# Kernel tuning notes

Hardware: AMD Instinct MI355X
Metric: run time of the kernel (lower is better)

## Reference

```python
import jax, jax.numpy as jnp
import numpy as np

N = 50000
E = 800000
H = 8
DH = 32  # hidden 256 / heads 8


def gat_layer(h, src, dst, W, a_src, a_dst, b):
    # h: [N, 256] -> per-head projected features [N, H, DH]
    hp = (h @ W).reshape(N, H, DH)
    # per-node attention logits for src/dst roles: [N, H]
    s_src = jnp.einsum('nhd,hd->nh', hp, a_src)
    s_dst = jnp.einsum('nhd,hd->nh', hp, a_dst)
    e = jax.nn.leaky_relu(s_src[src] + s_dst[dst], negative_slope=0.2)  # [Et, H]
    # segment softmax over incoming edges of each dst node
    m = jax.ops.segment_max(e, dst, num_segments=N)  # [N, H]
    ex = jnp.exp(e - m[dst])
    denom = jax.ops.segment_sum(ex, dst, num_segments=N)  # [N, H] (>0: self-loops)
    alpha = ex / denom[dst]  # [Et, H]
    out = jax.ops.segment_sum(alpha[:, :, None] * hp[src], dst, num_segments=N)
    return out.reshape(N, H * DH) + b


def han_forward(x, edges, proj_W, proj_b, gat_W, gat_asrc, gat_adst, gat_b,
                sem_W1, sem_b1, sem_W2, cls_W1, cls_b1, cls_W2, cls_b2):
    h0 = x @ proj_W + proj_b  # [N, 256]
    loop = jnp.arange(N, dtype=edges.dtype)
    embs = []
    for p in range(edges.shape[0]):  # 3 meta-paths (fixed, small)
        src = jnp.concatenate([edges[p, 0], loop])  # add self-loops (PyG default)
        dst = jnp.concatenate([edges[p, 1], loop])
        h = h0
        for l in range(2):  # 2 GAT layers per meta-path
            h = gat_layer(h, src, dst, gat_W[p, l], gat_asrc[p, l], gat_adst[p, l], gat_b[p, l])
            h = jax.nn.elu(h)  # dropout: eval-mode no-op
        embs.append(h)
    emb = jnp.stack(embs, axis=1)  # [N, P, 256]
    scores = (jnp.tanh(emb @ sem_W1 + sem_b1) @ sem_W2).squeeze(-1)  # [N, P]
    w = jax.nn.softmax(scores, axis=1)
    z = jnp.sum(emb * w[:, :, None], axis=1)  # [N, 256]
    hcls = jax.nn.relu(z @ cls_W1 + cls_b1)
    logits = hcls @ cls_W2 + cls_b2  # [N, 2]
    return logits


def setup_inputs() -> dict:
    key = jax.random.key(0)
    ks = jax.random.split(key, 16)
    s = 0.05
    return {
        'x': jax.random.normal(ks[0], (N, 128), jnp.float32),
        'edges': jax.random.randint(ks[1], (3, 2, E), 0, N, dtype=jnp.int32),
        'proj_W': jax.random.normal(ks[2], (128, 256), jnp.float32) * s,
        'proj_b': jnp.zeros((256,), jnp.float32),
        'gat_W': jax.random.normal(ks[3], (3, 2, 256, 256), jnp.float32) * s,
        'gat_asrc': jax.random.normal(ks[4], (3, 2, H, DH), jnp.float32) * s,
        'gat_adst': jax.random.normal(ks[5], (3, 2, H, DH), jnp.float32) * s,
        'gat_b': jnp.zeros((3, 2, 256), jnp.float32),
        'sem_W1': jax.random.normal(ks[6], (256, 128), jnp.float32) * s,
        'sem_b1': jnp.zeros((128,), jnp.float32),
        'sem_W2': jax.random.normal(ks[7], (128, 1), jnp.float32) * s,
        'cls_W1': jax.random.normal(ks[8], (256, 128), jnp.float32) * s,
        'cls_b1': jnp.zeros((128,), jnp.float32),
        'cls_W2': jax.random.normal(ks[9], (128, 2), jnp.float32) * s,
        'cls_b2': jnp.zeros((2,), jnp.float32),
    }


def reference(x, edges, proj_W, proj_b, gat_W, gat_asrc, gat_adst, gat_b,
              sem_W1, sem_b1, sem_W2, cls_W1, cls_b1, cls_W2, cls_b2):
    return han_forward(x, edges, proj_W, proj_b, gat_W, gat_asrc, gat_adst, gat_b,
                       sem_W1, sem_b1, sem_W2, cls_W1, cls_b1, cls_W2, cls_b2)
```

## Files before the change

### kernel.cpp

```cpp
#include <hip/hip_runtime.h>
#include <hip/hip_fp16.h>
#include <math.h>

#define N_NODES 50000
#define N_EDG   800000
#define NH      8
#define DH      32
#define HID     256
#define MAXD    64
#define EPB     4096
#define PROJ_FB 88
#define PROJ_EB (176*EPB)
#define G3_FB   69

typedef __attribute__((ext_vector_type(8))) short bf16x8;
typedef __attribute__((ext_vector_type(4))) float f32x4;

__device__ __forceinline__ unsigned short f2bf(float x) {
    unsigned u = __float_as_uint(x);
    u += 0x7FFF + ((u >> 16) & 1);
    return (unsigned short)(u >> 16);
}
__device__ __forceinline__ float bf2f(unsigned short h) {
    return __uint_as_float(((unsigned)h) << 16);
}
__device__ __forceinline__ float fastrcp(float x) {
    float r;
    asm("v_rcp_f32 %0, %1" : "=v"(r) : "v"(x));
    return r;
}
__device__ __forceinline__ void split8(const float4& a, const float4& b,
                                       uint4& hi, uint4& lo) {
    float v[8] = {a.x,a.y,a.z,a.w,b.x,b.y,b.z,b.w};
    unsigned short h[8], l[8];
    #pragma unroll
    for (int i = 0; i < 8; ++i) { h[i] = f2bf(v[i]); l[i] = f2bf(v[i] - bf2f(h[i])); }
// ... 34 lines not shown
        int dd[4], ss[4];
        #pragma unroll
        for (int j = 0; j < 4; ++j) {
            int e = base + (t * 4 + j) * 256;
            if (e < 3 * N_EDG) {
                int p = e / N_EDG, i = e - p * N_EDG;
                const int* src = edges + (size_t)p * 2 * N_EDG;
                int s = src[i], d = src[N_EDG + i];
                ss[j] = min(max(s, 0), N_NODES - 1);
                dd[j] = p * N_NODES + min(max(d, 0), N_NODES - 1);
            } else { ss[j] = -1; dd[j] = 0; }
        }
        int pos[4];
        #pragma unroll
        for (int j = 0; j < 4; ++j)
            if (ss[j] >= 0) pos[j] = atomicAdd(&cnt3[dd[j]], 1);
        #pragma unroll
        for (int j = 0; j < 4; ++j)
            if (ss[j] >= 0 && pos[j] < MAXD)
                slots3[(size_t)dd[j] * MAXD + pos[j]] = (unsigned short)ss[j];
    }
}

template<int NC, int ACT, int OUTMODE, int AMODE, int FILL>
__global__ __launch_bounds__(256)
void mfma_gemm_k(const float* __restrict__ A32p, const __half* __restrict__ A16p,
                 int lda,
                 const unsigned short* __restrict__ WThi,
                 const unsigned short* __restrict__ WTlo,
                 const float* __restrict__ bias,
                 float* __restrict__ C, __half* __restrict__ Ch,
                 int ldc, int M, int K,
                 const int* __restrict__ edges, int* __restrict__ cnt3,
                 unsigned short* __restrict__ slots3) {
    __shared__ unsigned short sAh[128*32], sAl[128*32], sBh[128*32], sBl[128*32];
    if constexpr (FILL) {
        const int gxk = (M + 127) >> 7;
        if ((int)blockIdx.x >= gxk) {
            fill_edges(edges, cnt3, slots3,
                       ((int)blockIdx.x - gxk) + PROJ_FB * (int)blockIdx.y, 0);
            return;
        }
    }
    const int tid  = threadIdx.x;
    const int lane = tid & 63;
    const int w    = tid >> 6;
    const int wr   = w >> 1, wc = w & 1;
    const int r0   = blockIdx.x * 128;
    const int c0   = blockIdx.y * 128;
    const int l15  = lane & 15, q = lane >> 4;

    const int cl8   = (((lane & 3) ^ ((lane >> 4) & 3)) << 3);
    const int lrow  = w*32 + (lane >> 2);
    const int gbrow0 = c0 + lrow, gbrow1 = c0 + lrow + 16;
    const int lbase = w * 1024;
    const int ldst  = lbase + lane * 8;

    const int srow = tid >> 2, slot = tid & 3;
    const size_t ga0 = (size_t)min(r0 + srow,      M - 1) * lda + slot * 8;
    const size_t ga1 = (size_t)min(r0 + srow + 64, M - 1) * lda + slot * 8;
    const int lda0 = srow*32 + ((slot ^ ((srow >> 2) & 3)) << 3);
    const int lda1 = lda0 + 64*32;

    f32x4 acc[4][4];
    #pragma unroll
    for (int i = 0; i < 4; ++i)
        #pragma unroll
        for (int j = 0; j < 4; ++j) acc[i][j] = (f32x4){0.f, 0.f, 0.f, 0.f};

    const int swzF = (l15 >> 2) & 3;
    const int qs   = ((q ^ swzF) << 3);

    const int nsteps = K >> 5;
    for (int s = 0; s < nsteps; ++s) {
        const int kc = s << 5;
        __syncthreads();
        uint4 h0, l0, h1, l1;
        if constexpr (AMODE == 0) {
            float4 f0a = *(const float4*)&A32p[ga0 + kc];
            float4 f0b = *(const float4*)&A32p[ga0 + kc + 4];
            float4 f1a = *(const float4*)&A32p[ga1 + kc];
            float4 f1b = *(const float4*)&A32p[ga1 + kc + 4];
            split8(f0a, f0b, h0, l0);
            split8(f1a, f1b, h1, l1);
        } else {
            uint4 r0v = *(const uint4*)&A16p[ga0 + kc];
            uint4 r1v = *(const uint4*)&A16p[ga1 + kc];
            h8_to_pair(r0v, h0, l0);
            h8_to_pair(r1v, h1, l1);
        }
        *(uint4*)&sAh[lda0] = h0; *(uint4*)&sAl[lda0] = l0;
        *(uint4*)&sAh[lda1] = h1; *(uint4*)&sAl[lda1] = l1;
        *(uint4*)&sBh[ldst]       = *(const uint4*)&WThi[(size_t)gbrow0*K + kc + cl8];
        *(uint4*)&sBh[ldst + 512] = *(const uint4*)&WThi[(size_t)gbrow1*K + kc + cl8];
        *(uint4*)&sBl[ldst]       = *(const uint4*)&WTlo[(size_t)gbrow0*K + kc + cl8];
        *(uint4*)&sBl[ldst + 512] = *(const uint4*)&WTlo[(size_t)gbrow1*K + kc + cl8];
        __syncthreads();

        bf16x8 fAh[4], fAl[4];
        #pragma unroll
        for (int t = 0; t < 4; ++t) {
            int ra = (wr*64 + t*16 + l15) * 32 + qs;
            fAh[t] = *(const bf16x8*)&sAh[ra];
            fAl[t] = *(const bf16x8*)&sAl[ra];
        }
        #pragma unroll
        for (int nt = 0; nt < 4; ++nt) {
            int rb = (wc*64 + nt*16 + l15) * 32 + qs;
            bf16x8 fBh = *(const bf16x8*)&sBh[rb];
            bf16x8 fBl = *(const bf16x8*)&sBl[rb];
            #pragma unroll
            for (int mt = 0; mt < 4; ++mt) {
                acc[mt][nt] = __builtin_amdgcn_mfma_f32_16x16x32_bf16(fAh[mt], fBh, acc[mt][nt], 0, 0, 0);
                acc[mt][nt] = __builtin_amdgcn_mfma_f32_16x16x32_bf16(fAh[mt], fBl, acc[mt][nt], 0, 0, 0);
                acc[mt][nt] = __builtin_amdgcn_mfma_f32_16x16x32_bf16(fAl[mt], fBh, acc[mt][nt], 0, 0, 0);
            }
        }
    }
    #pragma unroll
    for (int mt = 0; mt < 4; ++mt)
        #pragma unroll
        for (int nt = 0; nt < 4; ++nt) {
            int col = c0 + wc*64 + nt*16 + l15;
            float bb = bias ? bias[col] : 0.f;
            #pragma unroll
            for (int r = 0; r < 4; ++r) {
                int grow = r0 + wr*64 + mt*16 + q*4 + r;
                if (grow < M) {
                    float v = acc[mt][nt][r] + bb;
                    if (ACT == 1) {
                        float t = __expf(2.f * v);
                        v = 1.f - 2.f * fastrcp(1.f + t);
                    } else if (ACT == 2) v = fmaxf(v, 0.f);
                    size_t o = (size_t)grow * ldc + col;
                    if (OUTMODE == 2) Ch[o] = __float2half(v);
                    else              C[o] = v;
                }
            }
        }
}

template<int FILL>
__global__ __launch_bounds__(256)
void mfma_gemm3_k(const __half* __restrict__ A16p, int aoffz, int lda,
                  const unsigned short* __restrict__ WT, int l,
                  __half* __restrict__ hp3, int M,
                  const int* __restrict__ edges, int* __restrict__ cnt3,
                  unsigned short* __restrict__ slots3) {
    __shared__ unsigned short sAh[128*32], sAl[128*32], sBh[128*32], sBl[128*32];
    const int gx = (M + 127) >> 7;
    if constexpr (FILL) {
        if ((int)blockIdx.x >= gx) {
            fill_edges(edges, cnt3, slots3,
                       ((int)blockIdx.x - gx) + G3_FB * ((int)blockIdx.y + 2 * (int)blockIdx.z),
                       PROJ_EB);
            return;
        }
    }
    const int p = blockIdx.z;
    A16p += (size_t)p * aoffz;
    const unsigned short* WThi = WT + (size_t)(2*p + l) * 131072;
    const unsigned short* WTlo = WThi + 65536;
    __half* Ch = hp3 + (size_t)p * N_NODES * HID;
    const int K = HID;

    const int tid  = threadIdx.x;
    const int lane = tid & 63;
    const int w    = tid >> 6;
    const int wr   = w >> 1, wc = w & 1;
    const int r0   = blockIdx.x * 128;
    const int c0   = blockIdx.y * 128;
    const int l15  = lane & 15, q = lane >> 4;

    const int cl8   = (((lane & 3) ^ ((lane >> 4) & 3)) << 3);
    const int lrow  = w*32 + (lane >> 2);
    const int gbrow0 = c0 + lrow, gbrow1 = c0 + lrow + 16;
    const int lbase = w * 1024;
    const int ldst  = lbase + lane * 8;

    const int srow = tid >> 2, slot = tid & 3;
    const size_t ga0 = (size_t)min(r0 + srow,      M - 1) * lda + slot * 8;
    const size_t ga1 = (size_t)min(r0 + srow + 64, M - 1) * lda + slot * 8;
    const int lda0 = srow*32 + ((slot ^ ((srow >> 2) & 3)) << 3);
    const int lda1 = lda0 + 64*32;

    f32x4 acc[4][4];
    #pragma unroll
    for (int i = 0; i < 4; ++i)
        #pragma unroll
        for (int j = 0; j < 4; ++j) acc[i][j] = (f32x4){0.f, 0.f, 0.f, 0.f};

    const int swzF = (l15 >> 2) & 3;
    const int qs   = ((q ^ swzF) << 3);

    for (int s = 0; s < 8; ++s) {
        const int kc = s << 5;
        __syncthreads();
        uint4 r0v = *(const uint4*)&A16p[ga0 + kc];
        uint4 r1v = *(const uint4*)&A16p[ga1 + kc];
        uint4 h0, l0, h1, l1;
        h8_to_pair(r0v, h0, l0);
        h8_to_pair(r1v, h1, l1);
        *(uint4*)&sAh[lda0] = h0; *(uint4*)&sAl[lda0] = l0;
        *(uint4*)&sAh[lda1] = h1; *(uint4*)&sAl[lda1] = l1;
        *(uint4*)&sBh[ldst]       = *(const uint4*)&WThi[(size_t)gbrow0*K + kc + cl8];
        *(uint4*)&sBh[ldst + 512] = *(const uint4*)&WThi[(size_t)gbrow1*K + kc + cl8];
        *(uint4*)&sBl[ldst]       = *(const uint4*)&WTlo[(size_t)gbrow0*K + kc + cl8];
        *(uint4*)&sBl[ldst + 512] = *(const uint4*)&WTlo[(size_t)gbrow1*K + kc + cl8];
        __syncthreads();

        bf16x8 fAh[4], fAl[4];
        #pragma unroll
        for (int t = 0; t < 4; ++t) {
            int ra = (wr*64 + t*16 + l15) * 32 + qs;
            fAh[t] = *(const bf16x8*)&sAh[ra];
            fAl[t] = *(const bf16x8*)&sAl[ra];
        }
        #pragma unroll
        for (int nt = 0; nt < 4; ++nt) {
            int rb = (wc*64 + nt*16 + l15) * 32 + qs;
            bf16x8 fBh = *(const bf16x8*)&sBh[rb];
            bf16x8 fBl = *(const bf16x8*)&sBl[rb];
            #pragma unroll
            for (int mt = 0; mt < 4; ++mt) {
                acc[mt][nt] = __builtin_amdgcn_mfma_f32_16x16x32_bf16(fAh[mt], fBh, acc[mt][nt], 0, 0, 0);
                acc[mt][nt] = __builtin_amdgcn_mfma_f32_16x16x32_bf16(fAh[mt], fBl, acc[mt][nt], 0, 0, 0);
                acc[mt][nt] = __builtin_amdgcn_mfma_f32_16x16x32_bf16(fAl[mt], fBh, acc[mt][nt], 0, 0, 0);
            }
        }
    }
    #pragma unroll
    for (int mt = 0; mt < 4; ++mt)
        #pragma unroll
        for (int nt = 0; nt < 4; ++nt) {
            int col = c0 + wc*64 + nt*16 + l15;
            #pragma unroll
            for (int r = 0; r < 4; ++r) {
                int grow = r0 + wr*64 + mt*16 + q*4 + r;
                if (grow < M)
                    Ch[(size_t)grow * HID + col] = __float2half(acc[mt][nt][r]);
            }
        }
}

__global__ __launch_bounds__(256)
void cvtWall_k(const float* __restrict__ gatW, const float* __restrict__ projW,
               const float* __restrict__ semW1, const float* __restrict__ clsW1,
               unsigned short* __restrict__ WT) {
    int y = blockIdx.y;
    const float* W; int K, N;
    if (y < 6)       { W = gatW + (size_t)y * 65536; K = 256; N = 256; }
    else if (y == 6) { W = projW; K = 128; N = 256; }
    else if (y == 7) { W = semW1; K = 256; N = 128; }
    else             { W = clsW1; K = 256; N = 128; }
    int idx = blockIdx.x * 256 + threadIdx.x;
    if (idx >= K * N) return;
    unsigned short* hi = WT + (size_t)y * 131072;
    unsigned short* lo = hi + 65536;
    int k = idx / N, n = idx - k * N;
    float v = W[idx];
    unsigned short h = f2bf(v);
    hi[n * K + k] = h;
    lo[n * K + k] = f2bf(v - bf2f(h));
}

__global__ __launch_bounds__(256)
void attn_scores3_k(const __half* __restrict__ hp3,
                    const float* __restrict__ gatAs, const float* __restrict__ gatAd,
                    int l, float* __restrict__ ssrc3, float* __restrict__ sdst3) {
    int p = blockIdx.y;
    int gid = blockIdx.x * 256 + threadIdx.x;
    if (gid >= N_NODES * NH) return;
    int h = gid & 7;
    const __half2* hv = (const __half2*)(hp3 + (size_t)p * N_NODES * HID + (size_t)gid * DH);
    const float* a = gatAs + (2*p + l) * HID + h * DH;
    const float* d = gatAd + (2*p + l) * HID + h * DH;
    float ss = 0.f, sd = 0.f;
    #pragma unroll
    for (int j = 0; j < 8; ++j) {
        float4 av = ((const float4*)a)[j], dv = ((const float4*)d)[j];
        float2 f0 = __half22float2(hv[2*j]);
        float2 f1 = __half22float2(hv[2*j + 1]);
        ss += f0.x*av.x + f0.y*av.y + f1.x*av.z + f1.y*av.w;
        sd += f0.x*dv.x + f0.y*dv.y + f1.x*dv.z + f1.y*dv.w;
    }
    ssrc3[p * N_NODES * NH + gid] = ss;
    sdst3[p * N_NODES * NH + gid] = sd;
}

__global__ __launch_bounds__(256)
void zero_k(int* p, int n) { int i = blockIdx.x*256 + threadIdx.x; if (i < n) p[i] = 0; }

__global__ __launch_bounds__(256)
void agg3_k(const int* __restrict__ cnt3, const unsigned short* __restrict__ slots3,
            const float* __restrict__ ssrc3, const float* __restrict__ sdst3,
            const __half* __restrict__ hp3, const float* __restrict__ gatB, int l,
            __half* __restrict__ emb16) {
    const int p = blockIdx.y;
    int wid  = (blockIdx.x * blockDim.x + threadIdx.x) >> 6;
    int lane = threadIdx.x & 63;
    if (wid >= N_NODES) return;
    const int n = wid;
    const unsigned short* srcs = slots3 + ((size_t)p * N_NODES + n) * MAXD;
    const float* s_src = ssrc3 + p * N_NODES * NH;
    const float* s_dst = sdst3 + p * N_NODES * NH;
    const __half* hp = hp3 + (size_t)p * N_NODES * HID;
    const float* bias = gatB + (2*p + l) * HID;
    const int deg = min(cnt3[p * N_NODES + n], MAXD);

    const int sub = lane & 31, eo = lane >> 5;
    const int h2  = sub >> 2;
    const float sd2 = s_dst[n*NH + h2];
    const uint4* hp4 = (const uint4*)hp;
    float dn = 0.f;
    float a0=0.f,a1=0.f,a2=0.f,a3=0.f,a4=0.f,a5=0.f,a6=0.f,a7=0.f;

    int i = eo;
    for (; i + 6 < deg; i += 8) {
        const int s0 = srcs[i];
        const int s1 = srcs[i + 2];
        const int s2 = srcs[i + 4];
        const int s3 = srcs[i + 6];
        const float x0 = s_src[s0*NH + h2];
// ... 52 lines not shown
    a4 += __shfl_xor(a4, 32); a5 += __shfl_xor(a5, 32);
    a6 += __shfl_xor(a6, 32); a7 += __shfl_xor(a7, 32);
    if (lane < 32) {
        float evs = s_src[n*NH + h2] + sd2;
        evs = evs > 0.f ? evs : 0.2f * evs;
        float ws = __expf(evs);
        dn += ws;
        const uint4 rs = hp4[n*32 + sub];
        fmix2(a0, a1, rs.x, ws); fmix2(a2, a3, rs.y, ws);
        fmix2(a4, a5, rs.z, ws); fmix2(a6, a7, rs.w, ws);

        float rdn = fastrcp(dn);
        float v[8] = {a0,a1,a2,a3,a4,a5,a6,a7};
        const float4 b0 = *(const float4*)&bias[sub*8];
        const float4 b1 = *(const float4*)&bias[sub*8 + 4];
        v[0]=v[0]*rdn+b0.x; v[1]=v[1]*rdn+b0.y; v[2]=v[2]*rdn+b0.z; v[3]=v[3]*rdn+b0.w;
        v[4]=v[4]*rdn+b1.x; v[5]=v[5]*rdn+b1.y; v[6]=v[6]*rdn+b1.z; v[7]=v[7]*rdn+b1.w;
        unsigned short hh[8];
        #pragma unroll
        for (int k = 0; k < 8; ++k) {
            float e = v[k] > 0.f ? v[k] : (__expf(v[k]) - 1.f);
            hh[k] = __half_as_ushort(__float2half(e));
        }
        size_t o = (size_t)n * 768 + p * HID + sub * 8;
        *(uint4*)&emb16[o] = make_uint4(hh[0]|((unsigned)hh[1]<<16), hh[2]|((unsigned)hh[3]<<16),
                                        hh[4]|((unsigned)hh[5]<<16), hh[6]|((unsigned)hh[7]<<16));
    }
}

__global__ __launch_bounds__(256)
void score_z_k(const float* t, const float* __restrict__ W2,
               const __half* __restrict__ emb16, float* z) {
    int wid  = (blockIdx.x * blockDim.x + threadIdx.x) >> 6;
    int lane = threadIdx.x & 63;
    if (wid >= N_NODES) return;
    const int n = wid;
    float sc[3];
    #pragma unroll
    for (int p = 0; p < 3; ++p) {
        const float* tr = t + (size_t)(n*3 + p) * 128;
        float part = tr[lane] * W2[lane] + tr[64 + lane] * W2[64 + lane];
        #pragma unroll
        for (int o = 1; o < 64; o <<= 1) part += __shfl_xor(part, o);
        sc[p] = part;
    }
    float m  = fmaxf(sc[0], fmaxf(sc[1], sc[2]));
    float e0 = __expf(sc[0]-m), e1 = __expf(sc[1]-m), e2 = __expf(sc[2]-m);
    float rs = fastrcp(e0 + e1 + e2);
    e0 *= rs; e1 *= rs; e2 *= rs;
    const __half* er = emb16 + (size_t)n * 768;
    for (int c = lane; c < 256; c += 64) {
        float v0 = __half2float(er[c]);
        float v1 = __half2float(er[256 + c]);
        float v2 = __half2float(er[512 + c]);
        z[(size_t)n*384 + c] = e0*v0 + e1*v1 + e2*v2;
    }
}

__global__ __launch_bounds__(256)
void logits_k(const float* __restrict__ hcls, const float* __restrict__ W2,
              const float* __restrict__ b2, float* __restrict__ out) {
    int gid = blockIdx.x*256 + threadIdx.x;
    if (gid >= N_NODES * 2) return;
    int n = gid >> 1, o = gid & 1;
    const float* hr = hcls + (size_t)n * 128;
    float a = b2[o];
    #pragma unroll 4
    for (int j = 0; j < 128; ++j) a += hr[j] * W2[j*2 + o];
    out[gid] = a;
}

extern "C" void kernel_launch(void* const* d_in, const int* in_sizes, int n_in,
                              void* d_out, int out_size, void* d_ws, size_t ws_size,
                              hipStream_t stream) {
    (void)in_sizes; (void)n_in; (void)out_size; (void)ws_size;
    const float* x     = (const float*)d_in[0];
    const int*   edges = (const int*)  d_in[1];
    const float* projW = (const float*)d_in[2];
    const float* projb = (const float*)d_in[3];
// ... 1 lines not shown
    const float* gatAs = (const float*)d_in[5];
    const float* gatAd = (const float*)d_in[6];
    const float* gatB  = (const float*)d_in[7];
    const float* semW1 = (const float*)d_in[8];
    const float* semb1 = (const float*)d_in[9];
    const float* semW2 = (const float*)d_in[10];
    const float* clsW1 = (const float*)d_in[11];
    const float* clsb1 = (const float*)d_in[12];
    const float* clsW2 = (const float*)d_in[13];
    const float* clsb2 = (const float*)d_in[14];
    float* out = (float*)d_out;

    char* base = (char*)d_ws;
    const size_t PLANE = (size_t)N_NODES * HID * 2;
    __half* hp3   = (__half*)(base);
    __half* emb16 = (__half*)(base + 3*PLANE);
    __half* h016  = (__half*)(base + 6*PLANE);
    char* small = base + 7*PLANE;
    float* ssrc3 = (float*)small;
    float* sdst3 = ssrc3 + 3*(size_t)N_NODES*NH;
    int*   cnt3  = (int*)(sdst3 + 3*(size_t)N_NODES*NH);
    unsigned short* WT = (unsigned short*)(cnt3 + 3*N_NODES);
    unsigned short* slots3 = WT + 9*131072;
    float* tbuf = (float*)base;
    float* hcls = (float*)(base + 6*PLANE);

    dim3 blk(256);
    const int gx = (N_NODES + 127) / 128;

    cvtWall_k<<<dim3(256, 9), blk, 0, stream>>>(gatW, projW, semW1, clsW1, WT);
    zero_k  <<<(3*N_NODES+255)/256, blk, 0, stream>>>(cnt3, 3*N_NODES);

    mfma_gemm_k<256,0,2,0,1><<<dim3(gx + PROJ_FB, 2), blk, 0, stream>>>(
        x, nullptr, 128, WT + 6*131072, WT + 6*131072 + 65536, projb,
        nullptr, h016, 256, N_NODES, 128, edges, cnt3, slots3);

    for (int l = 0; l < 2; ++l) {
        if (l == 0)
            mfma_gemm3_k<1><<<dim3(gx + G3_FB, 2, 3), blk, 0, stream>>>(
                h016, 0, HID, WT, 0, hp3, N_NODES, edges, cnt3, slots3);
        else
            mfma_gemm3_k<0><<<dim3(gx, 2, 3), blk, 0, stream>>>(
                emb16, HID, 3*HID, WT, 1, hp3, N_NODES, edges, cnt3, slots3);
        attn_scores3_k<<<dim3((N_NODES*NH+255)/256, 3), blk, 0, stream>>>(
            hp3, gatAs, gatAd, l, ssrc3, sdst3);
        agg3_k<<<dim3((N_NODES*64)/256, 3), blk, 0, stream>>>(
            cnt3, slots3, ssrc3, sdst3, hp3, gatB, l, emb16);
    }

    mfma_gemm_k<128,1,0,1,0><<<dim3((150000+127)/128, 1), blk, 0, stream>>>(
        nullptr, emb16, 256, WT + 7*131072, WT + 7*131072 + 65536, semb1,
        tbuf, nullptr, 128, 150000, 256, nullptr, nullptr, nullptr);
    score_z_k<<<(N_NODES*64)/256, blk, 0, stream>>>(tbuf, semW2, emb16, tbuf);
    mfma_gemm_k<128,2,0,0,0><<<dim3(gx, 1), blk, 0, stream>>>(
        tbuf, nullptr, 384, WT + 8*131072, WT + 8*131072 + 65536, clsb1,
        hcls, nullptr, 128, N_NODES, 256, nullptr, nullptr, nullptr);
    logits_k<<<(N_NODES*2+255)/256, blk, 0, stream>>>(hcls, clsW2, clsb2, out);
}
```

Baseline: 984.2 us.

## Overlap per-metapath aggregation with GEMMs and fuse semantic weighting into classifier load

Breaks the batched three-metapath layer loop into per-metapath launches so each aggregation runs as extra blocks inside the next metapath's projection GEMM or semantic GEMM. This overlaps gather-heavy aggregation with MFMA work. The embedding layout changes from interleaved per-node to planar per-metapath. The semantic score kernel now writes only three softmax weights per node, and the classifier GEMM forms the weighted sum of the three embeddings while loading its A tile, which removes the z buffer write and read. The cost is more launches and heterogeneous blocks sharing one kernel, which can hurt occupancy or the balance of work across blocks.

```diff
diff --git a/kernel.cpp b/kernel.cpp
--- a/kernel.cpp
+++ b/kernel.cpp
@@ -12,6 +12,8 @@
 #define PROJ_FB 88
 #define PROJ_EB (176*EPB)
 #define G3_FB   69
+#define AGGB    12500
+#define AGGX3   6250
 
 typedef __attribute__((ext_vector_type(8))) short bf16x8;
 typedef __attribute__((ext_vector_type(4))) float f32x4;
@@ -92,283 +94,14 @@
     }
 }
 
-template<int NC, int ACT, int OUTMODE, int AMODE, int FILL>
-__global__ __launch_bounds__(256)
-void mfma_gemm_k(const float* __restrict__ A32p, const __half* __restrict__ A16p,
-                 int lda,
-                 const unsigned short* __restrict__ WThi,
-                 const unsigned short* __restrict__ WTlo,
-                 const float* __restrict__ bias,
-                 float* __restrict__ C, __half* __restrict__ Ch,
-                 int ldc, int M, int K,
-                 const int* __restrict__ edges, int* __restrict__ cnt3,
-                 unsigned short* __restrict__ slots3) {
-    __shared__ unsigned short sAh[128*32], sAl[128*32], sBh[128*32], sBl[128*32];
-    if constexpr (FILL) {
-        const int gxk = (M + 127) >> 7;
-        if ((int)blockIdx.x >= gxk) {
-            fill_edges(edges, cnt3, slots3,
-                       ((int)blockIdx.x - gxk) + PROJ_FB * (int)blockIdx.y, 0);
-            return;
-        }
-    }
-    const int tid  = threadIdx.x;
-    const int lane = tid & 63;
-    const int w    = tid >> 6;
-    const int wr   = w >> 1, wc = w & 1;
-    const int r0   = blockIdx.x * 128;
-    const int c0   = blockIdx.y * 128;
-    const int l15  = lane & 15, q = lane >> 4;
-
-    const int cl8   = (((lane & 3) ^ ((lane >> 4) & 3)) << 3);
-    const int lrow  = w*32 + (lane >> 2);
-    const int gbrow0 = c0 + lrow, gbrow1 = c0 + lrow + 16;
-    const int lbase = w * 1024;
-    const int ldst  = lbase + lane * 8;
-
-    const int srow = tid >> 2, slot = tid & 3;
-    const size_t ga0 = (size_t)min(r0 + srow,      M - 1) * lda + slot * 8;
-    const size_t ga1 = (size_t)min(r0 + srow + 64, M - 1) * lda + slot * 8;
-    const int lda0 = srow*32 + ((slot ^ ((srow >> 2) & 3)) << 3);
-    const int lda1 = lda0 + 64*32;
-
-    f32x4 acc[4][4];
-    #pragma unroll
-    for (int i = 0; i < 4; ++i)
-        #pragma unroll
-        for (int j = 0; j < 4; ++j) acc[i][j] = (f32x4){0.f, 0.f, 0.f, 0.f};
-
-    const int swzF = (l15 >> 2) & 3;
-    const int qs   = ((q ^ swzF) << 3);
-
-    const int nsteps = K >> 5;
-    for (int s = 0; s < nsteps; ++s) {
-        const int kc = s << 5;
-        __syncthreads();
-        uint4 h0, l0, h1, l1;
-        if constexpr (AMODE == 0) {
-            float4 f0a = *(const float4*)&A32p[ga0 + kc];
-            float4 f0b = *(const float4*)&A32p[ga0 + kc + 4];
-            float4 f1a = *(const float4*)&A32p[ga1 + kc];
-            float4 f1b = *(const float4*)&A32p[ga1 + kc + 4];
-            split8(f0a, f0b, h0, l0);
-            split8(f1a, f1b, h1, l1);
-        } else {
-            uint4 r0v = *(const uint4*)&A16p[ga0 + kc];
-            uint4 r1v = *(const uint4*)&A16p[ga1 + kc];
-            h8_to_pair(r0v, h0, l0);
-            h8_to_pair(r1v, h1, l1);
-        }
-        *(uint4*)&sAh[lda0] = h0; *(uint4*)&sAl[lda0] = l0;
-        *(uint4*)&sAh[lda1] = h1; *(uint4*)&sAl[lda1] = l1;
-        *(uint4*)&sBh[ldst]       = *(const uint4*)&WThi[(size_t)gbrow0*K + kc + cl8];
-        *(uint4*)&sBh[ldst + 512] = *(const uint4*)&WThi[(size_t)gbrow1*K + kc + cl8];
-        *(uint4*)&sBl[ldst]       = *(const uint4*)&WTlo[(size_t)gbrow0*K + kc + cl8];
-        *(uint4*)&sBl[ldst + 512] = *(const uint4*)&WTlo[(size_t)gbrow1*K + kc + cl8];
-        __syncthreads();
-
-        bf16x8 fAh[4], fAl[4];
-        #pragma unroll
-        for (int t = 0; t < 4; ++t) {
-            int ra = (wr*64 + t*16 + l15) * 32 + qs;
-            fAh[t] = *(const bf16x8*)&sAh[ra];
-            fAl[t] = *(const bf16x8*)&sAl[ra];
-        }
-        #pragma unroll
-        for (int nt = 0; nt < 4; ++nt) {
-            int rb = (wc*64 + nt*16 + l15) * 32 + qs;
-            bf16x8 fBh = *(const bf16x8*)&sBh[rb];
-            bf16x8 fBl = *(const bf16x8*)&sBl[rb];
-            #pragma unroll
-            for (int mt = 0; mt < 4; ++mt) {
-                acc[mt][nt] = __builtin_amdgcn_mfma_f32_16x16x32_bf16(fAh[mt], fBh, acc[mt][nt], 0, 0, 0);
-                acc[mt][nt] = __builtin_amdgcn_mfma_f32_16x16x32_bf16(fAh[mt], fBl, acc[mt][nt], 0, 0, 0);
-                acc[mt][nt] = __builtin_amdgcn_mfma_f32_16x16x32_bf16(fAl[mt], fBh, acc[mt][nt], 0, 0, 0);
-            }
-        }
-    }
-    #pragma unroll
-    for (int mt = 0; mt < 4; ++mt)
-        #pragma unroll
-        for (int nt = 0; nt < 4; ++nt) {
-            int col = c0 + wc*64 + nt*16 + l15;
-            float bb = bias ? bias[col] : 0.f;
-            #pragma unroll
-            for (int r = 0; r < 4; ++r) {
-                int grow = r0 + wr*64 + mt*16 + q*4 + r;
-                if (grow < M) {
-                    float v = acc[mt][nt][r] + bb;
-                    if (ACT == 1) {
-                        float t = __expf(2.f * v);
-                        v = 1.f - 2.f * fastrcp(1.f + t);
-                    } else if (ACT == 2) v = fmaxf(v, 0.f);
-                    size_t o = (size_t)grow * ldc + col;
-                    if (OUTMODE == 2) Ch[o] = __float2half(v);
-                    else              C[o] = v;
-                }
-            }
-        }
-}
-
-template<int FILL>
-__global__ __launch_bounds__(256)
-void mfma_gemm3_k(const __half* __restrict__ A16p, int aoffz, int lda,
-                  const unsigned short* __restrict__ WT, int l,
-                  __half* __restrict__ hp3, int M,
-                  const int* __restrict__ edges, int* __restrict__ cnt3,
-                  unsigned short* __restrict__ slots3) {
-    __shared__ unsigned short sAh[128*32], sAl[128*32], sBh[128*32], sBl[128*32];
-    const int gx = (M + 127) >> 7;
-    if constexpr (FILL) {
-        if ((int)blockIdx.x >= gx) {
-            fill_edges(edges, cnt3, slots3,
-                       ((int)blockIdx.x - gx) + G3_FB * ((int)blockIdx.y + 2 * (int)blockIdx.z),
-                       PROJ_EB);
-            return;
-        }
-    }
-    const int p = blockIdx.z;
-    A16p += (size_t)p * aoffz;
-    const unsigned short* WThi = WT + (size_t)(2*p + l) * 131072;
-    const unsigned short* WTlo = WThi + 65536;
-    __half* Ch = hp3 + (size_t)p * N_NODES * HID;
-    const int K = HID;
-
-    const int tid  = threadIdx.x;
-    const int lane = tid & 63;
-    const int w    = tid >> 6;
-    const int wr   = w >> 1, wc = w & 1;
-    const int r0   = blockIdx.x * 128;
-    const int c0   = blockIdx.y * 128;
-    const int l15  = lane & 15, q = lane >> 4;
-
-    const int cl8   = (((lane & 3) ^ ((lane >> 4) & 3)) << 3);
-    const int lrow  = w*32 + (lane >> 2);
-    const int gbrow0 = c0 + lrow, gbrow1 = c0 + lrow + 16;
-    const int lbase = w * 1024;
-    const int ldst  = lbase + lane * 8;
-
-    const int srow = tid >> 2, slot = tid & 3;
-    const size_t ga0 = (size_t)min(r0 + srow,      M - 1) * lda + slot * 8;
-    const size_t ga1 = (size_t)min(r0 + srow + 64, M - 1) * lda + slot * 8;
-    const int lda0 = srow*32 + ((slot ^ ((srow >> 2) & 3)) << 3);
-    const int lda1 = lda0 + 64*32;
-
-    f32x4 acc[4][4];
-    #pragma unroll
-    for (int i = 0; i < 4; ++i)
-        #pragma unroll
-        for (int j = 0; j < 4; ++j) acc[i][j] = (f32x4){0.f, 0.f, 0.f, 0.f};
-
-    const int swzF = (l15 >> 2) & 3;
-    const int qs   = ((q ^ swzF) << 3);
-
-    for (int s = 0; s < 8; ++s) {
-        const int kc = s << 5;
-        __syncthreads();
-        uint4 r0v = *(const uint4*)&A16p[ga0 + kc];
-        uint4 r1v = *(const uint4*)&A16p[ga1 + kc];
-        uint4 h0, l0, h1, l1;
-        h8_to_pair(r0v, h0, l0);
-        h8_to_pair(r1v, h1, l1);
-        *(uint4*)&sAh[lda0] = h0; *(uint4*)&sAl[lda0] = l0;
-        *(uint4*)&sAh[lda1] = h1; *(uint4*)&sAl[lda1] = l1;
-        *(uint4*)&sBh[ldst]       = *(const uint4*)&WThi[(size_t)gbrow0*K + kc + cl8];
-        *(uint4*)&sBh[ldst + 512] = *(const uint4*)&WThi[(size_t)gbrow1*K + kc + cl8];
-        *(uint4*)&sBl[ldst]       = *(const uint4*)&WTlo[(size_t)gbrow0*K + kc + cl8];
-        *(uint4*)&sBl[ldst + 512] = *(const uint4*)&WTlo[(size_t)gbrow1*K + kc + cl8];
-        __syncthreads();
-
-        bf16x8 fAh[4], fAl[4];
-        #pragma unroll
-        for (int t = 0; t < 4; ++t) {
-            int ra = (wr*64 + t*16 + l15) * 32 + qs;
-            fAh[t] = *(const bf16x8*)&sAh[ra];
-            fAl[t] = *(const bf16x8*)&sAl[ra];
-        }
-        #pragma unroll
-        for (int nt = 0; nt < 4; ++nt) {
-            int rb = (wc*64 + nt*16 + l15) * 32 + qs;
-            bf16x8 fBh = *(const bf16x8*)&sBh[rb];
-            bf16x8 fBl = *(const bf16x8*)&sBl[rb];
-            #pragma unroll
-            for (int mt = 0; mt < 4; ++mt) {
-                acc[mt][nt] = __builtin_amdgcn_mfma_f32_16x16x32_bf16(fAh[mt], fBh, acc[mt][nt], 0, 0, 0);
-                acc[mt][nt] = __builtin_amdgcn_mfma_f32_16x16x32_bf16(fAh[mt], fBl, acc[mt][nt], 0, 0, 0);
-                acc[mt][nt] = __builtin_amdgcn_mfma_f32_16x16x32_bf16(fAl[mt], fBh, acc[mt][nt], 0, 0, 0);
-            }
-        }
-    }
-    #pragma unroll
-    for (int mt = 0; mt < 4; ++mt)
-        #pragma unroll
-        for (int nt = 0; nt < 4; ++nt) {
-            int col = c0 + wc*64 + nt*16 + l15;
-            #pragma unroll
-            for (int r = 0; r < 4; ++r) {
-                int grow = r0 + wr*64 + mt*16 + q*4 + r;
-                if (grow < M)
-                    Ch[(size_t)grow * HID + col] = __float2half(acc[mt][nt][r]);
-            }
-        }
-}
-
-__global__ __launch_bounds__(256)
-void cvtWall_k(const float* __restrict__ gatW, const float* __restrict__ projW,
-               const float* __restrict__ semW1, const float* __restrict__ clsW1,
-               unsigned short* __restrict__ WT) {
-    int y = blockIdx.y;
-    const float* W; int K, N;
-    if (y < 6)       { W = gatW + (size_t)y * 65536; K = 256; N = 256; }
-    else if (y == 6) { W = projW; K = 128; N = 256; }
-    else if (y == 7) { W = semW1; K = 256; N = 128; }
-    else             { W = clsW1; K = 256; N = 128; }
-    int idx = blockIdx.x * 256 + threadIdx.x;
-    if (idx >= K * N) return;
-    unsigned short* hi = WT + (size_t)y * 131072;
-    unsigned short* lo = hi + 65536;
-    int k = idx / N, n = idx - k * N;
-    float v = W[idx];
-    unsigned short h = f2bf(v);
-    hi[n * K + k] = h;
-    lo[n * K + k] = f2bf(v - bf2f(h));
-}
-
-__global__ __launch_bounds__(256)
-void attn_scores3_k(const __half* __restrict__ hp3,
-                    const float* __restrict__ gatAs, const float* __restrict__ gatAd,
-                    int l, float* __restrict__ ssrc3, float* __restrict__ sdst3) {
-    int p = blockIdx.y;
-    int gid = blockIdx.x * 256 + threadIdx.x;
-    if (gid >= N_NODES * NH) return;
-    int h = gid & 7;
-    const __half2* hv = (const __half2*)(hp3 + (size_t)p * N_NODES * HID + (size_t)gid * DH);
-    const float* a = gatAs + (2*p + l) * HID + h * DH;
-    const float* d = gatAd + (2*p + l) * HID + h * DH;
-    float ss = 0.f, sd = 0.f;
-    #pragma unroll
-    for (int j = 0; j < 8; ++j) {
-        float4 av = ((const float4*)a)[j], dv = ((const float4*)d)[j];
-        float2 f0 = __half22float2(hv[2*j]);
-        float2 f1 = __half22float2(hv[2*j + 1]);
-        ss += f0.x*av.x + f0.y*av.y + f1.x*av.z + f1.y*av.w;
-        sd += f0.x*dv.x + f0.y*dv.y + f1.x*dv.z + f1.y*dv.w;
-    }
-    ssrc3[p * N_NODES * NH + gid] = ss;
-    sdst3[p * N_NODES * NH + gid] = sd;
-}
-
-__global__ __launch_bounds__(256)
-void zero_k(int* p, int n) { int i = blockIdx.x*256 + threadIdx.x; if (i < n) p[i] = 0; }
-
-__global__ __launch_bounds__(256)
-void agg3_k(const int* __restrict__ cnt3, const unsigned short* __restrict__ slots3,
-            const float* __restrict__ ssrc3, const float* __restrict__ sdst3,
-            const __half* __restrict__ hp3, const float* __restrict__ gatB, int l,
-            __half* __restrict__ emb16) {
-    const int p = blockIdx.y;
-    int wid  = (blockIdx.x * blockDim.x + threadIdx.x) >> 6;
-    int lane = threadIdx.x & 63;
+__device__ __forceinline__ void agg_worker(
+    int fb, int p, int l,
+    const int* __restrict__ cnt3, const unsigned short* __restrict__ slots3,
+    const float* __restrict__ ssrc3, const float* __restrict__ sdst3,
+    const __half* __restrict__ hp3, const float* __restrict__ gatB,
+    __half* __restrict__ emb16) {
+    const int wid  = fb * 4 + ((int)threadIdx.x >> 6);
+    const int lane = threadIdx.x & 63;
     if (wid >= N_NODES) return;
     const int n = wid;
     const unsigned short* srcs = slots3 + ((size_t)p * N_NODES + n) * MAXD;
@@ -467,15 +200,342 @@
             float e = v[k] > 0.f ? v[k] : (__expf(v[k]) - 1.f);
             hh[k] = __half_as_ushort(__float2half(e));
         }
-        size_t o = (size_t)n * 768 + p * HID + sub * 8;
+        size_t o = ((size_t)p * N_NODES + n) * HID + sub * 8;
         *(uint4*)&emb16[o] = make_uint4(hh[0]|((unsigned)hh[1]<<16), hh[2]|((unsigned)hh[3]<<16),
                                         hh[4]|((unsigned)hh[5]<<16), hh[6]|((unsigned)hh[7]<<16));
     }
 }
 
 __global__ __launch_bounds__(256)
-void score_z_k(const float* t, const float* __restrict__ W2,
-               const __half* __restrict__ emb16, float* z) {
+void agg1_k(const int* __restrict__ cnt3, const unsigned short* __restrict__ slots3,
+            const float* __restrict__ ssrc3, const float* __restrict__ sdst3,
+            const __half* __restrict__ hp3, const float* __restrict__ gatB,
+            int p, int l, __half* __restrict__ emb16) {
+    agg_worker(blockIdx.x, p, l, cnt3, slots3, ssrc3, sdst3, hp3, gatB, emb16);
+}
+
+template<int NC, int ACT, int OUTMODE, int AMODE, int FILL, int AGG>
+__global__ __launch_bounds__(256)
+void mfma_gemm_k(const float* __restrict__ A32p, const __half* __restrict__ A16p,
+                 int lda,
+                 const unsigned short* __restrict__ WThi,
+                 const unsigned short* __restrict__ WTlo,
+                 const float* __restrict__ bias,
+                 float* __restrict__ C, __half* __restrict__ Ch,
+                 int ldc, int M, int K,
+                 const int* __restrict__ edges, int* __restrict__ cnt3,
+                 unsigned short* __restrict__ slots3,
+                 const float* __restrict__ ssrc3, const float* __restrict__ sdst3,
+                 const float* __restrict__ gatB, const __half* __restrict__ aggHp,
+                 __half* __restrict__ aggEmb, int aggp, int aggl,
+                 const float* __restrict__ w4z) {
+    __shared__ unsigned short sAh[128*32], sAl[128*32], sBh[128*32], sBl[128*32];
+    const int gxk = (M + 127) >> 7;
+    if constexpr (FILL) {
+        if ((int)blockIdx.x >= gxk) {
+            fill_edges(edges, cnt3, slots3,
+                       ((int)blockIdx.x - gxk) + PROJ_FB * (int)blockIdx.y, 0);
+            return;
+        }
+    }
+    if constexpr (AGG) {
+        if ((int)blockIdx.x >= gxk) {
+            agg_worker((int)blockIdx.x - gxk, aggp, aggl,
+                       cnt3, slots3, ssrc3, sdst3, aggHp, gatB, aggEmb);
+            return;
+        }
+    }
+    const int tid  = threadIdx.x;
+    const int lane = tid & 63;
+    const int w    = tid >> 6;
+    const int wr   = w >> 1, wc = w & 1;
+    const int r0   = blockIdx.x * 128;
+    const int c0   = blockIdx.y * 128;
+    const int l15  = lane & 15, q = lane >> 4;
+
+    const int cl8   = (((lane & 3) ^ ((lane >> 4) & 3)) << 3);
+    const int lrow  = w*32 + (lane >> 2);
+    const int gbrow0 = c0 + lrow, gbrow1 = c0 + lrow + 16;
+    const int lbase = w * 1024;
+    const int ldst  = lbase + lane * 8;
+
+    const int srow = tid >> 2, slot = tid & 3;
+    const int arow0 = min(r0 + srow,      M - 1);
+    const int arow1 = min(r0 + srow + 64, M - 1);
+    const size_t ga0 = (size_t)arow0 * lda + slot * 8;
+    const size_t ga1 = (size_t)arow1 * lda + slot * 8;
+    const int lda0 = srow*32 + ((slot ^ ((srow >> 2) & 3)) << 3);
+    const int lda1 = lda0 + 64*32;
+
+    float4 w0r, w1r;
+    if constexpr (AMODE == 3) {
+        w0r = *(const float4*)&w4z[arow0 * 4];
+        w1r = *(const float4*)&w4z[arow1 * 4];
+    }
+
+    f32x4 acc[4][4];
+    #pragma unroll
+    for (int i = 0; i < 4; ++i)
+        #pragma unroll
+        for (int j = 0; j < 4; ++j) acc[i][j] = (f32x4){0.f, 0.f, 0.f, 0.f};
+
+    const int swzF = (l15 >> 2) & 3;
+    const int qs   = ((q ^ swzF) << 3);
+
+    const int nsteps = K >> 5;
+    for (int s = 0; s < nsteps; ++s) {
+        const int kc = s << 5;
+        __syncthreads();
+        uint4 h0, l0, h1, l1;
+        if constexpr (AMODE == 0) {
+            float4 f0a = *(const float4*)&A32p[ga0 + kc];
+            float4 f0b = *(const float4*)&A32p[ga0 + kc + 4];
+            float4 f1a = *(const float4*)&A32p[ga1 + kc];
+            float4 f1b = *(const float4*)&A32p[ga1 + kc + 4];
+            split8(f0a, f0b, h0, l0);
+            split8(f1a, f1b, h1, l1);
+        } else if constexpr (AMODE == 1) {
+            uint4 r0v = *(const uint4*)&A16p[ga0 + kc];
+            uint4 r1v = *(const uint4*)&A16p[ga1 + kc];
+            h8_to_pair(r0v, h0, l0);
+            h8_to_pair(r1v, h1, l1);
+        } else {
+            const int off = kc + slot * 8;
+            #pragma unroll
+            for (int rr = 0; rr < 2; ++rr) {
+                const int row = rr ? arow1 : arow0;
+                const float4 wv = rr ? w1r : w0r;
+                const __half2* e0 = (const __half2*)&A16p[(size_t)row * HID + off];
+                const __half2* e1 = (const __half2*)&A16p[((size_t)N_NODES + row) * HID + off];
+                const __half2* e2 = (const __half2*)&A16p[((size_t)2*N_NODES + row) * HID + off];
+                float vv[8];
+                #pragma unroll
+                for (int j2 = 0; j2 < 4; ++j2) {
+                    float2 fa = __half22float2(e0[j2]);
+                    float2 fb2 = __half22float2(e1[j2]);
+                    float2 fc = __half22float2(e2[j2]);
+                    vv[2*j2]   = wv.x*fa.x + wv.y*fb2.x + wv.z*fc.x;
+                    vv[2*j2+1] = wv.x*fa.y + wv.y*fb2.y + wv.z*fc.y;
+                }
+                if (rr) split8(*(const float4*)&vv[0], *(const float4*)&vv[4], h1, l1);
+                else    split8(*(const float4*)&vv[0], *(const float4*)&vv[4], h0, l0);
+            }
+        }
+        *(uint4*)&sAh[lda0] = h0; *(uint4*)&sAl[lda0] = l0;
+        *(uint4*)&sAh[lda1] = h1; *(uint4*)&sAl[lda1] = l1;
+        *(uint4*)&sBh[ldst]       = *(const uint4*)&WThi[(size_t)gbrow0*K + kc + cl8];
+        *(uint4*)&sBh[ldst + 512] = *(const uint4*)&WThi[(size_t)gbrow1*K + kc + cl8];
+        *(uint4*)&sBl[ldst]       = *(const uint4*)&WTlo[(size_t)gbrow0*K + kc + cl8];
+        *(uint4*)&sBl[ldst + 512] = *(const uint4*)&WTlo[(size_t)gbrow1*K + kc + cl8];
+        __syncthreads();
+
+        bf16x8 fAh[4], fAl[4];
+        #pragma unroll
+        for (int t = 0; t < 4; ++t) {
+            int ra = (wr*64 + t*16 + l15) * 32 + qs;
+            fAh[t] = *(const bf16x8*)&sAh[ra];
+            fAl[t] = *(const bf16x8*)&sAl[ra];
+        }
+        #pragma unroll
+        for (int nt = 0; nt < 4; ++nt) {
+            int rb = (wc*64 + nt*16 + l15) * 32 + qs;
+            bf16x8 fBh = *(const bf16x8*)&sBh[rb];
+            bf16x8 fBl = *(const bf16x8*)&sBl[rb];
+            #pragma unroll
+            for (int mt = 0; mt < 4; ++mt) {
+                acc[mt][nt] = __builtin_amdgcn_mfma_f32_16x16x32_bf16(fAh[mt], fBh, acc[mt][nt], 0, 0, 0);
+                acc[mt][nt] = __builtin_amdgcn_mfma_f32_16x16x32_bf16(fAh[mt], fBl, acc[mt][nt], 0, 0, 0);
+                acc[mt][nt] = __builtin_amdgcn_mfma_f32_16x16x32_bf16(fAl[mt], fBh, acc[mt][nt], 0, 0, 0);
+            }
+        }
+    }
+    #pragma unroll
+    for (int mt = 0; mt < 4; ++mt)
+        #pragma unroll
+        for (int nt = 0; nt < 4; ++nt) {
+            int col = c0 + wc*64 + nt*16 + l15;
+            float bb = bias ? bias[col] : 0.f;
+            #pragma unroll
+            for (int r = 0; r < 4; ++r) {
+                int grow = r0 + wr*64 + mt*16 + q*4 + r;
+                if (grow < M) {
+                    float v = acc[mt][nt][r] + bb;
+                    if (ACT == 1) {
+                        float t = __expf(2.f * v);
+                        v = 1.f - 2.f * fastrcp(1.f + t);
+                    } else if (ACT == 2) v = fmaxf(v, 0.f);
+                    size_t o = (size_t)grow * ldc + col;
+                    if (OUTMODE == 2) Ch[o] = __float2half(v);
+                    else              C[o] = v;
+                }
+            }
+        }
+}
+
+template<int FILL, int AGG>
+__global__ __launch_bounds__(256)
+void mfma_gemm3_k(const __half* __restrict__ A16p, int aoffz, int lda,
+                  const unsigned short* __restrict__ WT, int l,
+                  __half* __restrict__ hp3, int M, int pbase,
+                  const int* __restrict__ edges, int* __restrict__ cnt3,
+                  unsigned short* __restrict__ slots3,
+                  const float* __restrict__ ssrc3, const float* __restrict__ sdst3,
+                  const float* __restrict__ gatB, __half* __restrict__ aggEmb,
+                  int aggp, int aggl) {
+    __shared__ unsigned short sAh[128*32], sAl[128*32], sBh[128*32], sBl[128*32];
+    const int gx = (M + 127) >> 7;
+    if constexpr (FILL) {
+        if ((int)blockIdx.x >= gx) {
+            fill_edges(edges, cnt3, slots3,
+                       ((int)blockIdx.x - gx) + G3_FB * ((int)blockIdx.y + 2 * (int)blockIdx.z),
+                       PROJ_EB);
+            return;
+        }
+    }
+    if constexpr (AGG) {
+        if ((int)blockIdx.x >= gx) {
+            agg_worker(((int)blockIdx.x - gx) + AGGX3 * (int)blockIdx.y, aggp, aggl,
+                       cnt3, slots3, ssrc3, sdst3, hp3, gatB, aggEmb);
+            return;
+        }
+    }
+    const int p = pbase + blockIdx.z;
+    const __half* Ap = A16p + (size_t)p * aoffz;
+    const unsigned short* WThi = WT + (size_t)(2*p + l) * 131072;
+    const unsigned short* WTlo = WThi + 65536;
+    __half* Ch = hp3 + (size_t)p * N_NODES * HID;
+    const int K = HID;
+
+    const int tid  = threadIdx.x;
+    const int lane = tid & 63;
+    const int w    = tid >> 6;
+    const int wr   = w >> 1, wc = w & 1;
+    const int r0   = blockIdx.x * 128;
+    const int c0   = blockIdx.y * 128;
+    const int l15  = lane & 15, q = lane >> 4;
+
+    const int cl8   = (((lane & 3) ^ ((lane >> 4) & 3)) << 3);
+    const int lrow  = w*32 + (lane >> 2);
+    const int gbrow0 = c0 + lrow, gbrow1 = c0 + lrow + 16;
+    const int lbase = w * 1024;
+    const int ldst  = lbase + lane * 8;
+
+    const int srow = tid >> 2, slot = tid & 3;
+    const size_t ga0 = (size_t)min(r0 + srow,      M - 1) * lda + slot * 8;
+    const size_t ga1 = (size_t)min(r0 + srow + 64, M - 1) * lda + slot * 8;
+    const int lda0 = srow*32 + ((slot ^ ((srow >> 2) & 3)) << 3);
+    const int lda1 = lda0 + 64*32;
+
+    f32x4 acc[4][4];
+    #pragma unroll
+    for (int i = 0; i < 4; ++i)
+        #pragma unroll
+        for (int j = 0; j < 4; ++j) acc[i][j] = (f32x4){0.f, 0.f, 0.f, 0.f};
+
+    const int swzF = (l15 >> 2) & 3;
+    const int qs   = ((q ^ swzF) << 3);
+
+    for (int s = 0; s < 8; ++s) {
+        const int kc = s << 5;
+        __syncthreads();
+        uint4 r0v = *(const uint4*)&Ap[ga0 + kc];
+        uint4 r1v = *(const uint4*)&Ap[ga1 + kc];
+        uint4 h0, l0, h1, l1;
+        h8_to_pair(r0v, h0, l0);
+        h8_to_pair(r1v, h1, l1);
+        *(uint4*)&sAh[lda0] = h0; *(uint4*)&sAl[lda0] = l0;
+        *(uint4*)&sAh[lda1] = h1; *(uint4*)&sAl[lda1] = l1;
+        *(uint4*)&sBh[ldst]       = *(const uint4*)&WThi[(size_t)gbrow0*K + kc + cl8];
+        *(uint4*)&sBh[ldst + 512] = *(const uint4*)&WThi[(size_t)gbrow1*K + kc + cl8];
+        *(uint4*)&sBl[ldst]       = *(const uint4*)&WTlo[(size_t)gbrow0*K + kc + cl8];
+        *(uint4*)&sBl[ldst + 512] = *(const uint4*)&WTlo[(size_t)gbrow1*K + kc + cl8];
+        __syncthreads();
+
+        bf16x8 fAh[4], fAl[4];
+        #pragma unroll
+        for (int t = 0; t < 4; ++t) {
+            int ra = (wr*64 + t*16 + l15) * 32 + qs;
+            fAh[t] = *(const bf16x8*)&sAh[ra];
+            fAl[t] = *(const bf16x8*)&sAl[ra];
+        }
+        #pragma unroll
+        for (int nt = 0; nt < 4; ++nt) {
+            int rb = (wc*64 + nt*16 + l15) * 32 + qs;
+            bf16x8 fBh = *(const bf16x8*)&sBh[rb];
+            bf16x8 fBl = *(const bf16x8*)&sBl[rb];
+            #pragma unroll
+            for (int mt = 0; mt < 4; ++mt) {
+                acc[mt][nt] = __builtin_amdgcn_mfma_f32_16x16x32_bf16(fAh[mt], fBh, acc[mt][nt], 0, 0, 0);
+                acc[mt][nt] = __builtin_amdgcn_mfma_f32_16x16x32_bf16(fAh[mt], fBl, acc[mt][nt], 0, 0, 0);
+                acc[mt][nt] = __builtin_amdgcn_mfma_f32_16x16x32_bf16(fAl[mt], fBh, acc[mt][nt], 0, 0, 0);
+            }
+        }
+    }
+    #pragma unroll
+    for (int mt = 0; mt < 4; ++mt)
+        #pragma unroll
+        for (int nt = 0; nt < 4; ++nt) {
+            int col = c0 + wc*64 + nt*16 + l15;
+            #pragma unroll
+            for (int r = 0; r < 4; ++r) {
+                int grow = r0 + wr*64 + mt*16 + q*4 + r;
+                if (grow < M)
+                    Ch[(size_t)grow * HID + col] = __float2half(acc[mt][nt][r]);
+            }
+        }
+}
+
+__global__ __launch_bounds__(256)
+void cvtWall_k(const float* __restrict__ gatW, const float* __restrict__ projW,
+               const float* __restrict__ semW1, const float* __restrict__ clsW1,
+               unsigned short* __restrict__ WT) {
+    int y = blockIdx.y;
+    const float* W; int K, N;
+    if (y < 6)       { W = gatW + (size_t)y * 65536; K = 256; N = 256; }
+    else if (y == 6) { W = projW; K = 128; N = 256; }
+    else if (y == 7) { W = semW1; K = 256; N = 128; }
+    else             { W = clsW1; K = 256; N = 128; }
+    int idx = blockIdx.x * 256 + threadIdx.x;
+    if (idx >= K * N) return;
+    unsigned short* hi = WT + (size_t)y * 131072;
+    unsigned short* lo = hi + 65536;
+    int k = idx / N, n = idx - k * N;
+    float v = W[idx];
+    unsigned short h = f2bf(v);
+    hi[n * K + k] = h;
+    lo[n * K + k] = f2bf(v - bf2f(h));
+}
+
+__global__ __launch_bounds__(256)
+void attn_scores3_k(const __half* __restrict__ hp3,
+                    const float* __restrict__ gatAs, const float* __restrict__ gatAd,
+                    int l, int pbase, float* __restrict__ ssrc3, float* __restrict__ sdst3) {
+    int p = pbase + blockIdx.y;
+    int gid = blockIdx.x * 256 + threadIdx.x;
+    if (gid >= N_NODES * NH) return;
+    int h = gid & 7;
+    const __half2* hv = (const __half2*)(hp3 + (size_t)p * N_NODES * HID + (size_t)gid * DH);
+    const float* a = gatAs + (2*p + l) * HID + h * DH;
+    const float* d = gatAd + (2*p + l) * HID + h * DH;
+    float ss = 0.f, sd = 0.f;
+    #pragma unroll
+    for (int j = 0; j < 8; ++j) {
+        float4 av = ((const float4*)a)[j], dv = ((const float4*)d)[j];
+        float2 f0 = __half22float2(hv[2*j]);
+        float2 f1 = __half22float2(hv[2*j + 1]);
+        ss += f0.x*av.x + f0.y*av.y + f1.x*av.z + f1.y*av.w;
+        sd += f0.x*dv.x + f0.y*dv.y + f1.x*dv.z + f1.y*dv.w;
+    }
+    ssrc3[p * N_NODES * NH + gid] = ss;
+    sdst3[p * N_NODES * NH + gid] = sd;
+}
+
+__global__ __launch_bounds__(256)
+void zero_k(int* p, int n) { int i = blockIdx.x*256 + threadIdx.x; if (i < n) p[i] = 0; }
+
+__global__ __launch_bounds__(256)
+void score_w_k(const float* __restrict__ tb, const float* __restrict__ W2,
+               float* __restrict__ w4) {
     int wid  = (blockIdx.x * blockDim.x + threadIdx.x) >> 6;
     int lane = threadIdx.x & 63;
     if (wid >= N_NODES) return;
@@ -483,7 +543,7 @@
     float sc[3];
     #pragma unroll
     for (int p = 0; p < 3; ++p) {
-        const float* tr = t + (size_t)(n*3 + p) * 128;
+        const float* tr = tb + (size_t)p * N_NODES * 128 + (size_t)n * 128;
         float part = tr[lane] * W2[lane] + tr[64 + lane] * W2[64 + lane];
         #pragma unroll
         for (int o = 1; o < 64; o <<= 1) part += __shfl_xor(part, o);
@@ -492,14 +552,8 @@
     float m  = fmaxf(sc[0], fmaxf(sc[1], sc[2]));
     float e0 = __expf(sc[0]-m), e1 = __expf(sc[1]-m), e2 = __expf(sc[2]-m);
     float rs = fastrcp(e0 + e1 + e2);
-    e0 *= rs; e1 *= rs; e2 *= rs;
-    const __half* er = emb16 + (size_t)n * 768;
-    for (int c = lane; c < 256; c += 64) {
-        float v0 = __half2float(er[c]);
-        float v1 = __half2float(er[256 + c]);
-        float v2 = __half2float(er[512 + c]);
-        z[(size_t)n*384 + c] = e0*v0 + e1*v1 + e2*v2;
-    }
+    if (lane == 0)
+        *(float4*)&w4[(size_t)n * 4] = make_float4(e0*rs, e1*rs, e2*rs, 0.f);
 }
 
 __global__ __launch_bounds__(256)
@@ -547,7 +601,8 @@
     int*   cnt3  = (int*)(sdst3 + 3*(size_t)N_NODES*NH);
     unsigned short* WT = (unsigned short*)(cnt3 + 3*N_NODES);
     unsigned short* slots3 = WT + 9*131072;
-    float* tbuf = (float*)base;
+    float* w4 = (float*)(slots3 + (size_t)3*N_NODES*MAXD);
+    float* t0 = (float*)(base);
     float* hcls = (float*)(base + 6*PLANE);
 
     dim3 blk(256);
@@ -556,29 +611,59 @@
     cvtWall_k<<<dim3(256, 9), blk, 0, stream>>>(gatW, projW, semW1, clsW1, WT);
     zero_k  <<<(3*N_NODES+255)/256, blk, 0, stream>>>(cnt3, 3*N_NODES);
 
-    mfma_gemm_k<256,0,2,0,1><<<dim3(gx + PROJ_FB, 2), blk, 0, stream>>>(
+    mfma_gemm_k<256,0,2,0,1,0><<<dim3(gx + PROJ_FB, 2), blk, 0, stream>>>(
         x, nullptr, 128, WT + 6*131072, WT + 6*131072 + 65536, projb,
-        nullptr, h016, 256, N_NODES, 128, edges, cnt3, slots3);
-
-    for (int l = 0; l < 2; ++l) {
-        if (l == 0)
-            mfma_gemm3_k<1><<<dim3(gx + G3_FB, 2, 3), blk, 0, stream>>>(
-                h016, 0, HID, WT, 0, hp3, N_NODES, edges, cnt3, slots3);
-        else
-            mfma_gemm3_k<0><<<dim3(gx, 2, 3), blk, 0, stream>>>(
-                emb16, HID, 3*HID, WT, 1, hp3, N_NODES, edges, cnt3, slots3);
-        attn_scores3_k<<<dim3((N_NODES*NH+255)/256, 3), blk, 0, stream>>>(
-            hp3, gatAs, gatAd, l, ssrc3, sdst3);
-        agg3_k<<<dim3((N_NODES*64)/256, 3), blk, 0, stream>>>(
-            cnt3, slots3, ssrc3, sdst3, hp3, gatB, l, emb16);
-    }
-
-    mfma_gemm_k<128,1,0,1,0><<<dim3((150000+127)/128, 1), blk, 0, stream>>>(
+        nullptr, h016, 256, N_NODES, 128, edges, cnt3, slots3,
+        nullptr, nullptr, nullptr, nullptr, nullptr, 0, 0, nullptr);
+
+    mfma_gemm3_k<1,0><<<dim3(gx + G3_FB, 2, 3), blk, 0, stream>>>(
+        h016, 0, HID, WT, 0, hp3, N_NODES, 0, edges, cnt3, slots3,
+        nullptr, nullptr, nullptr, nullptr, 0, 0);
+
+    attn_scores3_k<<<dim3((N_NODES*NH+255)/256, 3), blk, 0, stream>>>(
+        hp3, gatAs, gatAd, 0, 0, ssrc3, sdst3);
+
+    agg1_k<<<dim3(AGGB), blk, 0, stream>>>(
+        cnt3, slots3, ssrc3, sdst3, hp3, gatB, 0, 0, emb16);
+
+    mfma_gemm3_k<0,1><<<dim3(gx + AGGX3, 2, 1), blk, 0, stream>>>(
+        emb16, (int)((size_t)N_NODES*HID), HID, WT, 1, hp3, N_NODES, 0,
+        nullptr, cnt3, slots3, ssrc3, sdst3, gatB, emb16, 1, 0);
+    mfma_gemm3_k<0,1><<<dim3(gx + AGGX3, 2, 1), blk, 0, stream>>>(
+        emb16, (int)((size_t)N_NODES*HID), HID, WT, 1, hp3, N_NODES, 1,
+        nullptr, cnt3, slots3, ssrc3, sdst3, gatB, emb16, 2, 0);
+
+    attn_scores3_k<<<dim3((N_NODES*NH+255)/256, 2), blk, 0, stream>>>(
+        hp3, gatAs, gatAd, 1, 0, ssrc3, sdst3);
+
+    mfma_gemm3_k<0,1><<<dim3(gx + AGGX3, 2, 1), blk, 0, stream>>>(
+        emb16, (int)((size_t)N_NODES*HID), HID, WT, 1, hp3, N_NODES, 2,
+        nullptr, cnt3, slots3, ssrc3, sdst3, gatB, emb16, 0, 1);
+
+    attn_scores3_k<<<dim3((N_NODES*NH+255)/256, 1), blk, 0, stream>>>(
+        hp3, gatAs, gatAd, 1, 2, ssrc3, sdst3);
+
+    mfma_gemm_k<128,1,0,1,0,1><<<dim3(gx + AGGB, 1), blk, 0, stream>>>(
         nullptr, emb16, 256, WT + 7*131072, WT + 7*131072 + 65536, semb1,
-        tbuf, nullptr, 128, 150000, 256, nullptr, nullptr, nullptr);
-    score_z_k<<<(N_NODES*64)/256, blk, 0, stream>>>(tbuf, semW2, emb16, tbuf);
-    mfma_gemm_k<128,2,0,0,0><<<dim3(gx, 1), blk, 0, stream>>>(
-        tbuf, nullptr, 384, WT + 8*131072, WT + 8*131072 + 65536, clsb1,
-        hcls, nullptr, 128, N_NODES, 256, nullptr, nullptr, nullptr);
+        t0, nullptr, 128, N_NODES, 256, nullptr, cnt3, slots3,
+        ssrc3, sdst3, gatB, hp3, emb16, 1, 1, nullptr);
+    mfma_gemm_k<128,1,0,1,0,1><<<dim3(gx + AGGB, 1), blk, 0, stream>>>(
+        nullptr, emb16 + (size_t)N_NODES*HID, 256,
+        WT + 7*131072, WT + 7*131072 + 65536, semb1,
+        t0 + (size_t)N_NODES*128, nullptr, 128, N_NODES, 256, nullptr, cnt3, slots3,
+        ssrc3, sdst3, gatB, hp3, emb16, 2, 1, nullptr);
+    mfma_gemm_k<128,1,0,1,0,0><<<dim3(gx, 1), blk, 0, stream>>>(
+        nullptr, emb16 + (size_t)2*N_NODES*HID, 256,
+        WT + 7*131072, WT + 7*131072 + 65536, semb1,
+        t0 + (size_t)2*N_NODES*128, nullptr, 128, N_NODES, 256, nullptr, nullptr, nullptr,
+        nullptr, nullptr, nullptr, nullptr, nullptr, 0, 0, nullptr);
+
+    score_w_k<<<dim3(AGGB), blk, 0, stream>>>(t0, semW2, w4);
+
+    mfma_gemm_k<128,2,0,3,0,0><<<dim3(gx, 1), blk, 0, stream>>>(
+        nullptr, emb16, HID, WT + 8*131072, WT + 8*131072 + 65536, clsb1,
+        hcls, nullptr, 128, N_NODES, 256, nullptr, nullptr, nullptr,
+        nullptr, nullptr, nullptr, nullptr, nullptr, 0, 0, w4);
+
     logits_k<<<(N_NODES*2+255)/256, blk, 0, stream>>>(hcls, clsW2, clsb2, out);
 }
```

Result: slower. 1.097 ms (+11.5%).
